# Optimization experiments

Measured on AMD Instinct MI355X. Metric: run time of the kernel, lower is better.

The kernel has to match this reference:

```python
import jax, jax.numpy as jnp
import numpy as np

B, T_IN, F_IN, H, T_OUT = 1024, 168, 8, 256, 96


def setup_inputs() -> dict:
    key = jax.random.key(0)
    ks = jax.random.split(key, 12)
    s = 1.0 / np.sqrt(H)  # torch LSTM/Linear default init scale
    return {
        "inputs": jax.random.normal(ks[0], (B, T_IN, F_IN), jnp.float32),
        "enc_Wih": jax.random.normal(ks[1], (4 * H, F_IN), jnp.float32) * s,
        "enc_Whh": jax.random.normal(ks[2], (4 * H, H), jnp.float32) * s,
        "enc_bih": jax.random.normal(ks[3], (4 * H,), jnp.float32) * s,
        "enc_bhh": jax.random.normal(ks[4], (4 * H,), jnp.float32) * s,
        "dec_Wih": jax.random.normal(ks[5], (4 * H, 1), jnp.float32) * s,
        "dec_Whh": jax.random.normal(ks[6], (4 * H, H), jnp.float32) * s,
        "dec_bih": jax.random.normal(ks[7], (4 * H,), jnp.float32) * s,
        "dec_bhh": jax.random.normal(ks[8], (4 * H,), jnp.float32) * s,
        "fc_W": jax.random.normal(ks[9], (1, H), jnp.float32) * s,
        "fc_b": jax.random.normal(ks[10], (1,), jnp.float32) * s,
    }


def _lstm_cell(x, h, c, Wih, Whh, bih, bhh):
    # PyTorch gate order: input, forget, cell(g), output
    gates = x @ Wih.T + h @ Whh.T + (bih + bhh)  # [B, 4H]
    i, f, g, o = jnp.split(gates, 4, axis=-1)
    c_new = jax.nn.sigmoid(f) * c + jax.nn.sigmoid(i) * jnp.tanh(g)
    h_new = jax.nn.sigmoid(o) * jnp.tanh(c_new)
    return h_new, c_new


def reference(inputs, enc_Wih, enc_Whh, enc_bih, enc_bhh,
              dec_Wih, dec_Whh, dec_bih, dec_bhh, fc_W, fc_b):
    batch = inputs.shape[0]
    hidden = inputs.shape[1] and enc_Whh.shape[1]
    h0 = jnp.zeros((batch, enc_Whh.shape[1]), inputs.dtype)
    c0 = jnp.zeros_like(h0)

    # ---- encoder: scan over input time steps ----
    def enc_step(carry, x_t):
        h, c = carry
        h, c = _lstm_cell(x_t, h, c, enc_Wih, enc_Whh, enc_bih, enc_bhh)
        return (h, c), None

    (h, c), _ = jax.lax.scan(enc_step, (h0, c0),
                             jnp.swapaxes(inputs, 0, 1))  # [T,B,F]

    x0 = inputs[:, -1, 0:1]  # [B,1] last value of main feature

    def dec_step(carry, _):
        x, h, c = carry
        h, c = _lstm_cell(x, h, c, dec_Wih, dec_Whh, dec_bih, dec_bhh)
        pred = h @ fc_W.T + fc_b  # [B,1]
        return (pred, h, c), pred

    _, preds = jax.lax.scan(dec_step, (x0, h, c), None, length=T_OUT)
    # preds: [T_OUT, B, 1] -> [B, T_OUT, 1]
    return jnp.swapaxes(preds, 0, 1)
```

## Files before the change

kernel.cpp:

```cpp
#include <hip/hip_runtime.h>


typedef _Float16 f16x8 __attribute__((ext_vector_type(8)));
typedef float f32x4 __attribute__((ext_vector_type(4)));

#define ROWP 296
#define WPW  36864
#define NSTEPS_ENC 168
#define NSTEPS_DEC 96

__device__ __forceinline__ float sigm(float x) {
    float e = __builtin_amdgcn_exp2f(-1.4426950408889634f * x);
    return __builtin_amdgcn_rcpf(1.0f + e);
}
__device__ __forceinline__ float tanh_f(float x) {
    float e = __builtin_amdgcn_exp2f(-2.8853900817779268f * x);
    return 2.0f * __builtin_amdgcn_rcpf(1.0f + e) - 1.0f;
}

__device__ __forceinline__ void step_gemm(f32x4 acc[8],
                                          const f16x8 wr[5][8],
                                          const f16x8 (*Bw)[64],
                                          const _Float16* __restrict__ wp,
                                          const _Float16 (*Ar)[ROWP],
                                          int lane, int l15, int lg) {
    f16x8 s7[8];
#pragma unroll
    for (int nt = 0; nt < 8; ++nt)
        s7[nt] = *(const f16x8*)(wp + ((7 * 8 + nt) * 64 + lane) * 8);

#pragma unroll
    for (int kt = 0; kt < 5; ++kt) {
        f16x8 a = *(const f16x8*)&Ar[l15][kt * 32 + lg * 8];
#pragma unroll
        for (int nt = 0; nt < 8; ++nt)
            acc[nt] = __builtin_amdgcn_mfma_f32_16x16x32_f16(a, wr[kt][nt], acc[nt], 0, 0, 0);
    }
    {
        f16x8 a = *(const f16x8*)&Ar[l15][7 * 32 + lg * 8];
#pragma unroll
        for (int nt = 0; nt < 8; ++nt)
            acc[nt] = __builtin_amdgcn_mfma_f32_16x16x32_f16(a, s7[nt], acc[nt], 0, 0, 0);
    }
    __builtin_amdgcn_sched_barrier(0);
    f16x8 s8[8];
#pragma unroll
    for (int nt = 0; nt < 8; ++nt)
        s8[nt] = *(const f16x8*)(wp + ((8 * 8 + nt) * 64 + lane) * 8);
#pragma unroll
    for (int kt = 5; kt < 7; ++kt) {
        f16x8 a = *(const f16x8*)&Ar[l15][kt * 32 + lg * 8];
#pragma unroll
        for (int nt = 0; nt < 8; ++nt) {
            f16x8 b = Bw[(kt - 5) * 8 + nt][lane];
            acc[nt] = __builtin_amdgcn_mfma_f32_16x16x32_f16(a, b, acc[nt], 0, 0, 0);
        }
    }
    {
        f16x8 a = *(const f16x8*)&Ar[l15][8 * 32 + lg * 8];
#pragma unroll
        for (int nt = 0; nt < 8; ++nt)
            acc[nt] = __builtin_amdgcn_mfma_f32_16x16x32_f16(a, s8[nt], acc[nt], 0, 0, 0);
    }
}

__device__ __forceinline__ void load_phase(f16x8 wr[5][8], f16x8 (*Bw)[64],
                                           const _Float16* __restrict__ wp,
                                           float* __restrict__ bL,
                                           const float* __restrict__ bias,
                                           int lane, int wv, int l15) {
#pragma unroll
    for (int kt = 0; kt < 5; ++kt)
#pragma unroll
        for (int nt = 0; nt < 8; ++nt)
            wr[kt][nt] = *(const f16x8*)(wp + ((kt * 8 + nt) * 64 + lane) * 8);
#pragma unroll
    for (int kt = 5; kt < 7; ++kt)
#pragma unroll
        for (int nt = 0; nt < 8; ++nt)
            Bw[(kt - 5) * 8 + nt][lane] = *(const f16x8*)(wp + ((kt * 8 + nt) * 64 + lane) * 8);
    if (lane < 16) {
#pragma unroll
        for (int nt = 0; nt < 8; ++nt)
            bL[wv * 128 + l15 * 8 + nt] = bias[(nt >> 1) * 256 + wv * 32 + (nt & 1) * 16 + l15];
    }
}


__global__ void k_convert_x(const float* __restrict__ in, _Float16* __restrict__ xf16) {
    int idx = blockIdx.x * 256 + threadIdx.x;
    if (idx >= 168 * 1024 * 8) return;
    int f = idx & 7;
    int b = (idx >> 3) & 1023;
    int t = idx >> 13;
    xf16[idx] = (_Float16)in[(b * 168 + t) * 8 + f];
}

__global__ void k_pack_w(const float* __restrict__ Whh, const float* __restrict__ Wih,
                         int IN, _Float16* __restrict__ Wp) {
    int idx = blockIdx.x * 256 + threadIdx.x;
    if (idx >= 294912) return;
    int j    = idx & 7;
    int lane = (idx >> 3) & 63;
    int nt   = (idx >> 9) & 7;
    int kt   = (idx >> 12) % 9;
    int wv   = idx / 36864;
    int n = (nt >> 1) * 256 + wv * 32 + (nt & 1) * 16 + (lane & 15);
    int k = kt * 32 + (lane >> 4) * 8 + j;
    float v = 0.0f;
    if (k < 256)            v = Whh[n * 256 + k];
    else if (k - 256 < IN)  v = Wih[n * IN + (k - 256)];
    Wp[idx] = (_Float16)v;
}


__global__ __launch_bounds__(512, 2) void lstm_seq2seq(
    const _Float16* __restrict__ xf16,
    const _Float16* __restrict__ WpE,
    const _Float16* __restrict__ WpD,
    const float* __restrict__ bihE, const float* __restrict__ bhhE,
    const float* __restrict__ bihD, const float* __restrict__ bhhD,
    const float* __restrict__ fcW,
    const float* __restrict__ fcb,
    float* __restrict__ out) {

    __shared__ f16x8 Blds[8][16][64];
    __shared__ _Float16 A[2][16][ROWP];
    __shared__ float partial[8][16];
    __shared__ float bL[8 * 128];

    const int tid = threadIdx.x;
    const int lane = tid & 63;
    const int wv  = tid >> 6;
    const int l15 = lane & 15;
    const int lg  = lane >> 4;
    const int b0  = blockIdx.x * 16;

    for (int i = tid; i < 2 * 16 * ROWP; i += 512)
        (&A[0][0][0])[i] = (_Float16)0.0f;

    f16x8 wr[5][8];
    const _Float16* wpe = WpE + wv * WPW;
    const _Float16* wpd = WpD + wv * WPW;

    if (lane < 16) {
#pragma unroll
        for (int nt = 0; nt < 8; ++nt) {
            int n = (nt >> 1) * 256 + wv * 32 + (nt & 1) * 16 + l15;
            bL[wv * 128 + l15 * 8 + nt] = bihE[n] + bhhE[n];
        }
    }
#pragma unroll
    for (int kt = 0; kt < 5; ++kt)
#pragma unroll
        for (int nt = 0; nt < 8; ++nt)
            wr[kt][nt] = *(const f16x8*)(wpe + ((kt * 8 + nt) * 64 + lane) * 8);
#pragma unroll
    for (int kt = 5; kt < 7; ++kt)
#pragma unroll
        for (int nt = 0; nt < 8; ++nt)
            Blds[wv][(kt - 5) * 8 + nt][lane] = *(const f16x8*)(wpe + ((kt * 8 + nt) * 64 + lane) * 8);

    float c_st[2][4] = {{0.f,0.f,0.f,0.f},{0.f,0.f,0.f,0.f}};

    __syncthreads();
    if (tid < 128) {
        int m = tid >> 3, f = tid & 7;
        A[0][m][256 + f] = xf16[(size_t)(b0 + m) * 8 + f];
    }
    __syncthreads();

#pragma unroll 1
    for (int t = 0; t < NSTEPS_ENC; ++t) {
        const int R = t & 1, Wb = R ^ 1;
        f32x4 bb0 = *(const f32x4*)&bL[wv * 128 + l15 * 8];
        f32x4 bb1 = *(const f32x4*)&bL[wv * 128 + l15 * 8 + 4];
        f32x4 acc[8];
#pragma unroll
        for (int nt = 0; nt < 8; ++nt) {
            float b = (nt < 4) ? bb0[nt & 3] : bb1[nt & 3];
            f32x4 v = {b, b, b, b};
            acc[nt] = v;
        }
        step_gemm(acc, wr, Blds[wv], wpe, A[R], lane, l15, lg);

#pragma unroll
        for (int half = 0; half < 2; ++half) {
#pragma unroll
            for (int r = 0; r < 4; ++r) {
                float iv = acc[0 + half][r];
                float fv = acc[2 + half][r];
                float gv = acc[4 + half][r];
                float ov = acc[6 + half][r];
                float cn = sigm(fv) * c_st[half][r] + sigm(iv) * tanh_f(gv);
                c_st[half][r] = cn;
                float hn = sigm(ov) * tanh_f(cn);
                A[Wb][lg * 4 + r][wv * 32 + half * 16 + l15] = (_Float16)hn;
            }
        }
        if (t < NSTEPS_ENC - 1) {
            if (tid < 128) {
                int m = tid >> 3, f = tid & 7;
                A[Wb][m][256 + f] = xf16[(size_t)((t + 1) * 1024 + b0 + m) * 8 + f];
            }
        } else {
            if (tid < 16) {
                A[Wb][tid][256] = xf16[(size_t)(167 * 1024 + b0 + tid) * 8 + 0];
#pragma unroll
                for (int f = 1; f < 8; ++f) A[Wb][tid][256 + f] = (_Float16)0.0f;
            }
        }
        __syncthreads();
    }

    if (lane < 16) {
#pragma unroll
        for (int nt = 0; nt < 8; ++nt) {
            int n = (nt >> 1) * 256 + wv * 32 + (nt & 1) * 16 + l15;
            bL[wv * 128 + l15 * 8 + nt] = bihD[n] + bhhD[n];
        }
    }
#pragma unroll
    for (int kt = 0; kt < 5; ++kt)
#pragma unroll
        for (int nt = 0; nt < 8; ++nt)
            wr[kt][nt] = *(const f16x8*)(wpd + ((kt * 8 + nt) * 64 + lane) * 8);
#pragma unroll
    for (int kt = 5; kt < 7; ++kt)
#pragma unroll
        for (int nt = 0; nt < 8; ++nt)
            Blds[wv][(kt - 5) * 8 + nt][lane] = *(const f16x8*)(wpd + ((kt * 8 + nt) * 64 + lane) * 8);
    float fcw0 = fcW[wv * 32 + l15];
    float fcw1 = fcW[wv * 32 + 16 + l15];
    float fcbv = fcb[0];
    __syncthreads();

#pragma unroll 1
    for (int s = 0; s < NSTEPS_DEC; ++s) {
        const int R = s & 1, Wb = R ^ 1;
        f32x4 bb0 = *(const f32x4*)&bL[wv * 128 + l15 * 8];
        f32x4 bb1 = *(const f32x4*)&bL[wv * 128 + l15 * 8 + 4];
        f32x4 acc[8];
#pragma unroll
        for (int nt = 0; nt < 8; ++nt) {
            float b = (nt < 4) ? bb0[nt & 3] : bb1[nt & 3];
            f32x4 v = {b, b, b, b};
            acc[nt] = v;
        }
        step_gemm(acc, wr, Blds[wv], wpd, A[R], lane, l15, lg);

        float hnv[2][4];
#pragma unroll
        for (int half = 0; half < 2; ++half) {
#pragma unroll
            for (int r = 0; r < 4; ++r) {
                float iv = acc[0 + half][r];
                float fv = acc[2 + half][r];
                float gv = acc[4 + half][r];
                float ov = acc[6 + half][r];
                float cn = sigm(fv) * c_st[half][r] + sigm(iv) * tanh_f(gv);
                c_st[half][r] = cn;
                float hn = sigm(ov) * tanh_f(cn);
                hnv[half][r] = hn;
                A[Wb][lg * 4 + r][wv * 32 + half * 16 + l15] = (_Float16)hn;
            }
        }
#pragma unroll
        for (int r = 0; r < 4; ++r) {
            float pv = hnv[0][r] * fcw0 + hnv[1][r] * fcw1;
            pv += __shfl_xor(pv, 1);
            pv += __shfl_xor(pv, 2);
            pv += __shfl_xor(pv, 4);
            pv += __shfl_xor(pv, 8);
            if (l15 == 0) partial[wv][lg * 4 + r] = pv;
        }
        __syncthreads();
        if (tid < 16) {
            float pr = fcbv;
#pragma unroll
            for (int w = 0; w < 8; ++w) pr += partial[w][tid];
            out[(size_t)(b0 + tid) * 96 + s] = pr;
            A[Wb][tid][256] = (_Float16)pr;
        }
        __syncthreads();
    }
}


extern "C" void kernel_launch(void* const* d_in, const int* in_sizes, int n_in,
                              void* d_out, int out_size, void* d_ws, size_t ws_size,
                              hipStream_t stream) {
    const float* inputs  = (const float*)d_in[0];
    const float* enc_Wih = (const float*)d_in[1];
    const float* enc_Whh = (const float*)d_in[2];
    const float* enc_bih = (const float*)d_in[3];
    const float* enc_bhh = (const float*)d_in[4];
    const float* dec_Wih = (const float*)d_in[5];
    const float* dec_Whh = (const float*)d_in[6];
    const float* dec_bih = (const float*)d_in[7];
    const float* dec_bhh = (const float*)d_in[8];
    const float* fc_W    = (const float*)d_in[9];
    const float* fc_b    = (const float*)d_in[10];

    char* ws = (char*)d_ws;
    _Float16* xf16 = (_Float16*)(ws);
    _Float16* WpE  = (_Float16*)(ws + 2752512);
    _Float16* WpD  = (_Float16*)(ws + 2752512 + 589824);

    k_convert_x<<<dim3(5376), dim3(256), 0, stream>>>(inputs, xf16);
    k_pack_w<<<dim3(1152), dim3(256), 0, stream>>>(enc_Whh, enc_Wih, 8, WpE);
    k_pack_w<<<dim3(1152), dim3(256), 0, stream>>>(dec_Whh, dec_Wih, 1, WpD);

    lstm_seq2seq<<<dim3(64), dim3(512), 0, stream>>>(
        xf16, WpE, WpD, enc_bih, enc_bhh, dec_bih, dec_bhh, fc_W, fc_b, (float*)d_out);
}
```

Measured before the change: 1.213 ms.

## Single-buffer swizzled hidden state, split input K-tile, move bias to registers

```diff
diff --git a/kernel.cpp b/kernel.cpp
--- a/kernel.cpp
+++ b/kernel.cpp
@@ -4,7 +4,6 @@
 typedef _Float16 f16x8 __attribute__((ext_vector_type(8)));
 typedef float f32x4 __attribute__((ext_vector_type(4)));
 
-#define ROWP 296
 #define WPW  36864
 #define NSTEPS_ENC 168
 #define NSTEPS_DEC 96
@@ -18,71 +17,49 @@
     return 2.0f * __builtin_amdgcn_rcpf(1.0f + e) - 1.0f;
 }
 
-__device__ __forceinline__ void step_gemm(f32x4 acc[8],
-                                          const f16x8 wr[5][8],
-                                          const f16x8 (*Bw)[64],
-                                          const _Float16* __restrict__ wp,
-                                          const _Float16 (*Ar)[ROWP],
-                                          int lane, int l15, int lg) {
-    f16x8 s7[8];
+__device__ __forceinline__ void mfma8(f32x4 acc[8], f16x8 a, const f16x8 b[8]) {
 #pragma unroll
     for (int nt = 0; nt < 8; ++nt)
-        s7[nt] = *(const f16x8*)(wp + ((7 * 8 + nt) * 64 + lane) * 8);
+        acc[nt] = __builtin_amdgcn_mfma_f32_16x16x32_f16(a, b[nt], acc[nt], 0, 0, 0);
+}
+
+__device__ __forceinline__ void gemm_all(f32x4 acc[8],
+                                         const f16x8 wr[5][8],
+                                         const f16x8 (*Bw)[64],
+                                         const f16x8 (*K8w)[16],
+                                         const _Float16* __restrict__ wp,
+                                         const char* ab, int abase,
+                                         const _Float16* xsrow,
+                                         int lane, int l15, int lg) {
+    f16x8 s5[8];
+#pragma unroll
+    for (int nt = 0; nt < 8; ++nt)
+        s5[nt] = *(const f16x8*)(wp + ((5 * 8 + nt) * 64 + lane) * 8);
 
 #pragma unroll
     for (int kt = 0; kt < 5; ++kt) {
-        f16x8 a = *(const f16x8*)&Ar[l15][kt * 32 + lg * 8];
-#pragma unroll
-        for (int nt = 0; nt < 8; ++nt)
-            acc[nt] = __builtin_amdgcn_mfma_f32_16x16x32_f16(a, wr[kt][nt], acc[nt], 0, 0, 0);
+        f16x8 a = *(const f16x8*)(ab + abase + kt * 64);
+        mfma8(acc, a, wr[kt]);
     }
     {
-        f16x8 a = *(const f16x8*)&Ar[l15][7 * 32 + lg * 8];
-#pragma unroll
-        for (int nt = 0; nt < 8; ++nt)
-            acc[nt] = __builtin_amdgcn_mfma_f32_16x16x32_f16(a, s7[nt], acc[nt], 0, 0, 0);
-    }
-    __builtin_amdgcn_sched_barrier(0);
-    f16x8 s8[8];
-#pragma unroll
-    for (int nt = 0; nt < 8; ++nt)
-        s8[nt] = *(const f16x8*)(wp + ((8 * 8 + nt) * 64 + lane) * 8);
-#pragma unroll
-    for (int kt = 5; kt < 7; ++kt) {
-        f16x8 a = *(const f16x8*)&Ar[l15][kt * 32 + lg * 8];
+        f16x8 a = *(const f16x8*)(ab + abase + 5 * 64);
+        mfma8(acc, a, s5);
+    }
+#pragma unroll
+    for (int kt = 6; kt < 8; ++kt) {
+        f16x8 a = *(const f16x8*)(ab + abase + kt * 64);
+#pragma unroll
+        for (int nt = 0; nt < 8; ++nt)
+            acc[nt] = __builtin_amdgcn_mfma_f32_16x16x32_f16(a, Bw[(kt - 6) * 8 + nt][lane], acc[nt], 0, 0, 0);
+    }
+    {
+        f16x8 a = *(const f16x8*)xsrow;
+        _Float16 m = (_Float16)(lg == 0 ? 1.0f : 0.0f);
 #pragma unroll
         for (int nt = 0; nt < 8; ++nt) {
-            f16x8 b = Bw[(kt - 5) * 8 + nt][lane];
+            f16x8 b = K8w[nt][l15] * m;
             acc[nt] = __builtin_amdgcn_mfma_f32_16x16x32_f16(a, b, acc[nt], 0, 0, 0);
         }
-    }
-    {
-        f16x8 a = *(const f16x8*)&Ar[l15][8 * 32 + lg * 8];
-#pragma unroll
-        for (int nt = 0; nt < 8; ++nt)
-            acc[nt] = __builtin_amdgcn_mfma_f32_16x16x32_f16(a, s8[nt], acc[nt], 0, 0, 0);
-    }
-}
-
-__device__ __forceinline__ void load_phase(f16x8 wr[5][8], f16x8 (*Bw)[64],
-                                           const _Float16* __restrict__ wp,
-                                           float* __restrict__ bL,
-                                           const float* __restrict__ bias,
-                                           int lane, int wv, int l15) {
-#pragma unroll
-    for (int kt = 0; kt < 5; ++kt)
-#pragma unroll
-        for (int nt = 0; nt < 8; ++nt)
-            wr[kt][nt] = *(const f16x8*)(wp + ((kt * 8 + nt) * 64 + lane) * 8);
-#pragma unroll
-    for (int kt = 5; kt < 7; ++kt)
-#pragma unroll
-        for (int nt = 0; nt < 8; ++nt)
-            Bw[(kt - 5) * 8 + nt][lane] = *(const f16x8*)(wp + ((kt * 8 + nt) * 64 + lane) * 8);
-    if (lane < 16) {
-#pragma unroll
-        for (int nt = 0; nt < 8; ++nt)
-            bL[wv * 128 + l15 * 8 + nt] = bias[(nt >> 1) * 256 + wv * 32 + (nt & 1) * 16 + l15];
     }
 }
 
@@ -125,111 +102,125 @@
     float* __restrict__ out) {
 
     __shared__ f16x8 Blds[8][16][64];
-    __shared__ _Float16 A[2][16][ROWP];
+    __shared__ f16x8 K8[8][8][16];
+    __shared__ _Float16 Abuf[16 * 256];
+    __shared__ _Float16 xs[16][8];
     __shared__ float partial[8][16];
-    __shared__ float bL[8 * 128];
-
-    const int tid = threadIdx.x;
+
+    const int tid  = threadIdx.x;
     const int lane = tid & 63;
-    const int wv  = tid >> 6;
-    const int l15 = lane & 15;
-    const int lg  = lane >> 4;
-    const int b0  = blockIdx.x * 16;
-
-    for (int i = tid; i < 2 * 16 * ROWP; i += 512)
-        (&A[0][0][0])[i] = (_Float16)0.0f;
-
-    f16x8 wr[5][8];
+    const int wv   = tid >> 6;
+    const int l15  = lane & 15;
+    const int lg   = lane >> 4;
+    const int b0   = blockIdx.x * 16;
+
+    const char* ab = (const char*)Abuf;
+    const int abase = l15 * 512 + ((lg * 16) ^ ((l15 & 3) << 4));
+
+    for (int i = tid; i < 16 * 256; i += 512) Abuf[i] = (_Float16)0.0f;
+
     const _Float16* wpe = WpE + wv * WPW;
     const _Float16* wpd = WpD + wv * WPW;
 
+    f16x8 wr[5][8];
+#pragma unroll
+    for (int kt = 0; kt < 5; ++kt)
+#pragma unroll
+        for (int nt = 0; nt < 8; ++nt)
+            wr[kt][nt] = *(const f16x8*)(wpe + ((kt * 8 + nt) * 64 + lane) * 8);
+#pragma unroll
+    for (int kt = 6; kt < 8; ++kt)
+#pragma unroll
+        for (int nt = 0; nt < 8; ++nt)
+            Blds[wv][(kt - 6) * 8 + nt][lane] = *(const f16x8*)(wpe + ((kt * 8 + nt) * 64 + lane) * 8);
     if (lane < 16) {
 #pragma unroll
-        for (int nt = 0; nt < 8; ++nt) {
-            int n = (nt >> 1) * 256 + wv * 32 + (nt & 1) * 16 + l15;
-            bL[wv * 128 + l15 * 8 + nt] = bihE[n] + bhhE[n];
-        }
-    }
-#pragma unroll
-    for (int kt = 0; kt < 5; ++kt)
-#pragma unroll
-        for (int nt = 0; nt < 8; ++nt)
-            wr[kt][nt] = *(const f16x8*)(wpe + ((kt * 8 + nt) * 64 + lane) * 8);
-#pragma unroll
-    for (int kt = 5; kt < 7; ++kt)
-#pragma unroll
-        for (int nt = 0; nt < 8; ++nt)
-            Blds[wv][(kt - 5) * 8 + nt][lane] = *(const f16x8*)(wpe + ((kt * 8 + nt) * 64 + lane) * 8);
+        for (int nt = 0; nt < 8; ++nt)
+            K8[wv][nt][lane] = *(const f16x8*)(wpe + ((8 * 8 + nt) * 64 + lane) * 8);
+    }
+    float bia[8];
+#pragma unroll
+    for (int nt = 0; nt < 8; ++nt) {
+        int n = (nt >> 1) * 256 + wv * 32 + (nt & 1) * 16 + l15;
+        bia[nt] = bihE[n] + bhhE[n];
+    }
 
     float c_st[2][4] = {{0.f,0.f,0.f,0.f},{0.f,0.f,0.f,0.f}};
 
     __syncthreads();
     if (tid < 128) {
         int m = tid >> 3, f = tid & 7;
-        A[0][m][256 + f] = xf16[(size_t)(b0 + m) * 8 + f];
+        xs[m][f] = xf16[(size_t)(b0 + m) * 8 + f];
     }
     __syncthreads();
 
 #pragma unroll 1
     for (int t = 0; t < NSTEPS_ENC; ++t) {
-        const int R = t & 1, Wb = R ^ 1;
-        f32x4 bb0 = *(const f32x4*)&bL[wv * 128 + l15 * 8];
-        f32x4 bb1 = *(const f32x4*)&bL[wv * 128 + l15 * 8 + 4];
         f32x4 acc[8];
 #pragma unroll
-        for (int nt = 0; nt < 8; ++nt) {
-            float b = (nt < 4) ? bb0[nt & 3] : bb1[nt & 3];
-            f32x4 v = {b, b, b, b};
-            acc[nt] = v;
-        }
-        step_gemm(acc, wr, Blds[wv], wpe, A[R], lane, l15, lg);
-
+        for (int nt = 0; nt < 8; ++nt) { f32x4 z = {0.f,0.f,0.f,0.f}; acc[nt] = z; }
+
+        _Float16 xh = (_Float16)0.0f;
+        if (t < NSTEPS_ENC - 1 && tid < 128)
+            xh = xf16[(size_t)((t + 1) * 1024 + b0 + (tid >> 3)) * 8 + (tid & 7)];
+
+        gemm_all(acc, wr, Blds[wv], K8[wv], wpe, ab, abase, &xs[l15][0], lane, l15, lg);
+
+        float hnv[2][4];
 #pragma unroll
         for (int half = 0; half < 2; ++half) {
 #pragma unroll
             for (int r = 0; r < 4; ++r) {
-                float iv = acc[0 + half][r];
-                float fv = acc[2 + half][r];
-                float gv = acc[4 + half][r];
-                float ov = acc[6 + half][r];
+                float iv = acc[0 + half][r] + bia[0 + half];
+                float fv = acc[2 + half][r] + bia[2 + half];
+                float gv = acc[4 + half][r] + bia[4 + half];
+                float ov = acc[6 + half][r] + bia[6 + half];
                 float cn = sigm(fv) * c_st[half][r] + sigm(iv) * tanh_f(gv);
                 c_st[half][r] = cn;
-                float hn = sigm(ov) * tanh_f(cn);
-                A[Wb][lg * 4 + r][wv * 32 + half * 16 + l15] = (_Float16)hn;
+                hnv[half][r] = sigm(ov) * tanh_f(cn);
+            }
+        }
+        __syncthreads();
+#pragma unroll
+        for (int half = 0; half < 2; ++half) {
+#pragma unroll
+            for (int r = 0; r < 4; ++r) {
+                int row = lg * 4 + r;
+                int colb = (wv * 32 + half * 16 + l15) * 2;
+                *(_Float16*)((char*)Abuf + row * 512 + (colb ^ ((r & 3) << 4))) = (_Float16)hnv[half][r];
             }
         }
         if (t < NSTEPS_ENC - 1) {
-            if (tid < 128) {
-                int m = tid >> 3, f = tid & 7;
-                A[Wb][m][256 + f] = xf16[(size_t)((t + 1) * 1024 + b0 + m) * 8 + f];
-            }
+            if (tid < 128) xs[tid >> 3][tid & 7] = xh;
         } else {
             if (tid < 16) {
-                A[Wb][tid][256] = xf16[(size_t)(167 * 1024 + b0 + tid) * 8 + 0];
-#pragma unroll
-                for (int f = 1; f < 8; ++f) A[Wb][tid][256 + f] = (_Float16)0.0f;
+#pragma unroll
+                for (int f = 1; f < 8; ++f) xs[tid][f] = (_Float16)0.0f;
             }
         }
         __syncthreads();
     }
 
+#pragma unroll
+    for (int kt = 0; kt < 5; ++kt)
+#pragma unroll
+        for (int nt = 0; nt < 8; ++nt)
+            wr[kt][nt] = *(const f16x8*)(wpd + ((kt * 8 + nt) * 64 + lane) * 8);
+#pragma unroll
+    for (int kt = 6; kt < 8; ++kt)
+#pragma unroll
+        for (int nt = 0; nt < 8; ++nt)
+            Blds[wv][(kt - 6) * 8 + nt][lane] = *(const f16x8*)(wpd + ((kt * 8 + nt) * 64 + lane) * 8);
     if (lane < 16) {
 #pragma unroll
-        for (int nt = 0; nt < 8; ++nt) {
-            int n = (nt >> 1) * 256 + wv * 32 + (nt & 1) * 16 + l15;
-            bL[wv * 128 + l15 * 8 + nt] = bihD[n] + bhhD[n];
-        }
-    }
-#pragma unroll
-    for (int kt = 0; kt < 5; ++kt)
-#pragma unroll
-        for (int nt = 0; nt < 8; ++nt)
-            wr[kt][nt] = *(const f16x8*)(wpd + ((kt * 8 + nt) * 64 + lane) * 8);
-#pragma unroll
-    for (int kt = 5; kt < 7; ++kt)
-#pragma unroll
-        for (int nt = 0; nt < 8; ++nt)
-            Blds[wv][(kt - 5) * 8 + nt][lane] = *(const f16x8*)(wpd + ((kt * 8 + nt) * 64 + lane) * 8);
+        for (int nt = 0; nt < 8; ++nt)
+            K8[wv][nt][lane] = *(const f16x8*)(wpd + ((8 * 8 + nt) * 64 + lane) * 8);
+    }
+#pragma unroll
+    for (int nt = 0; nt < 8; ++nt) {
+        int n = (nt >> 1) * 256 + wv * 32 + (nt & 1) * 16 + l15;
+        bia[nt] = bihD[n] + bhhD[n];
+    }
     float fcw0 = fcW[wv * 32 + l15];
     float fcw1 = fcW[wv * 32 + 16 + l15];
     float fcbv = fcb[0];
@@ -237,32 +228,24 @@
 
 #pragma unroll 1
     for (int s = 0; s < NSTEPS_DEC; ++s) {
-        const int R = s & 1, Wb = R ^ 1;
-        f32x4 bb0 = *(const f32x4*)&bL[wv * 128 + l15 * 8];
-        f32x4 bb1 = *(const f32x4*)&bL[wv * 128 + l15 * 8 + 4];
         f32x4 acc[8];
 #pragma unroll
-        for (int nt = 0; nt < 8; ++nt) {
-            float b = (nt < 4) ? bb0[nt & 3] : bb1[nt & 3];
-            f32x4 v = {b, b, b, b};
-            acc[nt] = v;
-        }
-        step_gemm(acc, wr, Blds[wv], wpd, A[R], lane, l15, lg);
+        for (int nt = 0; nt < 8; ++nt) { f32x4 z = {0.f,0.f,0.f,0.f}; acc[nt] = z; }
+
+        gemm_all(acc, wr, Blds[wv], K8[wv], wpd, ab, abase, &xs[l15][0], lane, l15, lg);
 
         float hnv[2][4];
 #pragma unroll
         for (int half = 0; half < 2; ++half) {
 #pragma unroll
             for (int r = 0; r < 4; ++r) {
-                float iv = acc[0 + half][r];
-                float fv = acc[2 + half][r];
-                float gv = acc[4 + half][r];
-                float ov = acc[6 + half][r];
+                float iv = acc[0 + half][r] + bia[0 + half];
+                float fv = acc[2 + half][r] + bia[2 + half];
+                float gv = acc[4 + half][r] + bia[4 + half];
+                float ov = acc[6 + half][r] + bia[6 + half];
                 float cn = sigm(fv) * c_st[half][r] + sigm(iv) * tanh_f(gv);
                 c_st[half][r] = cn;
-                float hn = sigm(ov) * tanh_f(cn);
-                hnv[half][r] = hn;
-                A[Wb][lg * 4 + r][wv * 32 + half * 16 + l15] = (_Float16)hn;
+                hnv[half][r] = sigm(ov) * tanh_f(cn);
             }
         }
 #pragma unroll
@@ -275,12 +258,21 @@
             if (l15 == 0) partial[wv][lg * 4 + r] = pv;
         }
         __syncthreads();
+#pragma unroll
+        for (int half = 0; half < 2; ++half) {
+#pragma unroll
+            for (int r = 0; r < 4; ++r) {
+                int row = lg * 4 + r;
+                int colb = (wv * 32 + half * 16 + l15) * 2;
+                *(_Float16*)((char*)Abuf + row * 512 + (colb ^ ((r & 3) << 4))) = (_Float16)hnv[half][r];
+            }
+        }
         if (tid < 16) {
             float pr = fcbv;
 #pragma unroll
             for (int w = 0; w < 8; ++w) pr += partial[w][tid];
             out[(size_t)(b0 + tid) * 96 + s] = pr;
-            A[Wb][tid][256] = (_Float16)pr;
+            xs[tid][0] = (_Float16)pr;
         }
         __syncthreads();
     }
```

Result: faster. 1.123 ms (-7.4%).
